# Performance work log

Measured on AMD Instinct MI355X. Metric: run time of the kernel, lower is better.

Reference implementation:

```python
import jax, jax.numpy as jnp
import numpy as np

N = 50000
E = 600000
H = 128   # hidden_channels (input to decoder)
O = 128   # output_channels (LSTM hidden size)
S = 8     # seq_len


def setup_inputs() -> dict:
    key = jax.random.key(0)
    ks = jax.random.split(key, 10)
    x = jax.random.normal(ks[0], (N, H), dtype=jnp.float32)
    c = jax.random.normal(ks[1], (N, H), dtype=jnp.float32)
    edge_index = jax.random.randint(ks[2], (2, E), 0, N, dtype=jnp.int64)
    # GCNConv weights (PyG: out = norm_agg(x @ W) + b)
    sc = lambda fan_in: 1.0 / np.sqrt(fan_in)
    Wh = jax.random.uniform(ks[3], (H, O), jnp.float32, -sc(H), sc(H))
    bh = jnp.zeros((O,), jnp.float32)
    Wc = jax.random.uniform(ks[4], (H, O), jnp.float32, -sc(H), sc(H))
    bc = jnp.zeros((O,), jnp.float32)
    # per-timestep cell convs: GCNConv(H + O, 4*O)
    Wcell = jax.random.uniform(ks[5], (S, H + O, 4 * O), jnp.float32, -sc(H + O), sc(H + O))
    bcell = jnp.zeros((S, 4 * O), jnp.float32)
    return {"x": x, "c": c, "edge_index": edge_index,
            "Wh": Wh, "bh": bh, "Wc": Wc, "bc": bc,
            "Wcell": Wcell, "bcell": bcell}


def _gcn(feat, W, b, src, dst, dinv):
    # PyG GCNConv with default add_self_loops=True, edge_weight=None:
    # out = D^{-1/2}(A+I)D^{-1/2} (feat @ W) + b
    xw = feat @ W                                   # [N, C_out]
    norm = (dinv[src] * dinv[dst])[:, None]         # [E, 1]
    agg = jax.ops.segment_sum(xw[src] * norm, dst, num_segments=N)
    agg = agg + (dinv * dinv)[:, None] * xw         # self-loop term
    return agg + b


def reference(x, c, edge_index, Wh, bh, Wc, bc, Wcell, bcell):
    src = edge_index[0]
    dst = edge_index[1]
    # degree (with self-loops, unit edge weights); computed on target index
    deg = jax.ops.segment_sum(jnp.ones((E,), jnp.float32), dst, num_segments=N) + 1.0
    dinv = 1.0 / jnp.sqrt(deg)

    h_cur = _gcn(x, Wh, bh, src, dst, dinv)
    c_cur = _gcn(c, Wc, bc, src, dst, dinv)

    def step(carry, params):
        h, cs = carry
        W, b = params
        combined = jnp.concatenate([x, h], axis=1)          # [N, H+O]
        cc = _gcn(combined, W, b, src, dst, dinv)           # [N, 4O]
        cc_f, cc_i, cc_o, cc_g = jnp.split(cc, 4, axis=1)
        f = jax.nn.sigmoid(cc_f)
        i = jax.nn.sigmoid(cc_i)
        o = jax.nn.sigmoid(cc_o)
        g = jnp.tanh(cc_g)
        c_next = f * cs + i * g
        h_next = o * jnp.tanh(c_next)
        return (h_next, c_next), h_next

    (h_fin, c_fin), hs = jax.lax.scan(step, (h_cur, c_cur), (Wcell, bcell))
    return hs, (h_fin, c_fin)  # hs: [S, N, O]
```

## Files before the change

kernel.cpp:

```cpp
#include <hip/hip_runtime.h>
#include <hip/hip_bf16.h>
#include <hip/hip_fp16.h>
#include <cstddef>


#define TPB 256

typedef __attribute__((ext_vector_type(8))) short bf16x8;
typedef __attribute__((ext_vector_type(4))) float f32x4;

__device__ __forceinline__ float sigf(float x) {
    return 1.0f / (1.0f + __expf(-x));
}
__device__ __forceinline__ float tanhfast(float x) {
    return 1.0f - 2.0f / (__expf(2.0f * x) + 1.0f);
}


__global__ void k_hist(const int* __restrict__ dst, int* __restrict__ counts, int E) {
    int e = blockIdx.x * TPB + threadIdx.x;
    if (e < E) atomicAdd(&counts[dst[e]], 1);
}

__global__ void k_scan_block(const int* __restrict__ counts, int* __restrict__ offsets,
                             int* __restrict__ sums, int N) {
    __shared__ int s[TPB];
    int tid = threadIdx.x;
    int gid = blockIdx.x * TPB + tid;
    int v = (gid < N) ? counts[gid] : 0;
    s[tid] = v;
    __syncthreads();
    for (int d = 1; d < TPB; d <<= 1) {
        int t = (tid >= d) ? s[tid - d] : 0;
        __syncthreads();
        s[tid] += t;
        __syncthreads();
    }
    if (gid < N) offsets[gid] = s[tid] - v;
    if (tid == TPB - 1) sums[blockIdx.x] = s[tid];
}

__global__ void k_scan_tops(int* __restrict__ sums, int nb) {
    __shared__ int s[TPB];
    int tid = threadIdx.x;
    int v = (tid < nb) ? sums[tid] : 0;
    s[tid] = v;
    __syncthreads();
    for (int d = 1; d < TPB; d <<= 1) {
        int t = (tid >= d) ? s[tid - d] : 0;
        __syncthreads();
        s[tid] += t;
        __syncthreads();
    }
    if (tid < nb) sums[tid] = s[tid] - v;
}

__global__ void k_scan_finish(const int* __restrict__ counts, int* __restrict__ offsets,
                              const int* __restrict__ sums, int* __restrict__ cursor,
                              float* __restrict__ dinv, int N, int E) {
    int gid = blockIdx.x * TPB + threadIdx.x;
    if (gid < N) {
        int off = offsets[gid] + sums[blockIdx.x];
        offsets[gid] = off;
        cursor[gid]  = off;
        dinv[gid]    = rsqrtf((float)(counts[gid] + 1));
    }
    if (gid == 0) offsets[N] = E;
}

__global__ void k_csr_scatter(const int* __restrict__ src, const int* __restrict__ dst,
                              const float* __restrict__ dinv, int* __restrict__ cursor,
                              int2* __restrict__ csr_sw, int E) {
    int e = blockIdx.x * TPB + threadIdx.x;
    if (e >= E) return;
    int d = dst[e], s = src[e];
    int pos = atomicAdd(&cursor[d], 1);
    int2 r;
    r.x = s;
    r.y = __float_as_int(dinv[s] * dinv[d]);
    csr_sw[pos] = r;
}


__global__ void k_f32tof16(const float* __restrict__ in, __half* __restrict__ out, int n4) {
    int i = blockIdx.x * TPB + threadIdx.x;
    if (i >= n4) return;
    float4 v = ((const float4*)in)[i];
    __half2 lo = __floats2half2_rn(v.x, v.y);
    __half2 hi = __floats2half2_rn(v.z, v.w);
    ((__half2*)out)[2 * i]     = lo;
    ((__half2*)out)[2 * i + 1] = hi;
}


union HU { f32x4 v; __half2 h[4]; };

__global__ __launch_bounds__(TPB) void k_aggregate_h(
        const __half* __restrict__ feat, __hip_bfloat16* __restrict__ agg,
        const int* __restrict__ offsets, const int2* __restrict__ sw,
        const float* __restrict__ dinv, int N) {
    int node = blockIdx.x * 4 + (threadIdx.x >> 6);
    if (node >= N) return;
    int lane = threadIdx.x & 63;
    int g = lane >> 4, t = lane & 15;
    const f32x4* f4 = (const f32x4*)feat;
    float acc[8];
    #pragma unroll
    for (int j = 0; j < 8; ++j) acc[j] = 0.f;

    int b = offsets[node], e = offsets[node + 1];
    for (int k = b; k < e; k += 4) {
        int kk = k + g;
        int kkc = (kk < e) ? kk : (e - 1);
        int2 sv = sw[kkc];
        float w = (kk < e) ? __int_as_float(sv.y) : 0.f;
        HU u;
        u.v = f4[(size_t)sv.x * 16 + t];
        #pragma unroll
        for (int j = 0; j < 4; ++j) {
            float2 vv = __half22float2(u.h[j]);
            acc[2 * j]     = fmaf(w, vv.x, acc[2 * j]);
            acc[2 * j + 1] = fmaf(w, vv.y, acc[2 * j + 1]);
        }
    }
    #pragma unroll
    for (int j = 0; j < 8; ++j) {
        acc[j] += __shfl_xor(acc[j], 16);
        acc[j] += __shfl_xor(acc[j], 32);
    }
    if (g == 0) {
        float di = dinv[node];
        float w0 = di * di;
        HU u;
        u.v = f4[(size_t)node * 16 + t];
        union { f32x4 v; __hip_bfloat162 b2[4]; } o;
        #pragma unroll
        for (int j = 0; j < 4; ++j) {
            float2 vv = __half22float2(u.h[j]);
            float ox = fmaf(w0, vv.x, acc[2 * j]);
            float oy = fmaf(w0, vv.y, acc[2 * j + 1]);
            o.b2[j].x = __float2bfloat16(ox);
            o.b2[j].y = __float2bfloat16(oy);
        }
        *(f32x4*)(agg + (size_t)node * 128 + t * 8) = o.v;
    }
}

__global__ __launch_bounds__(TPB) void k_aggregate_h2(
        const __half* __restrict__ fa, const __half* __restrict__ fb,
        __hip_bfloat16* __restrict__ aggA, __hip_bfloat16* __restrict__ aggB,
        const int* __restrict__ offsets, const int2* __restrict__ sw,
        const float* __restrict__ dinv, int N) {
    int node = blockIdx.x * 4 + (threadIdx.x >> 6);
    if (node >= N) return;
    int lane = threadIdx.x & 63;
    int g = lane >> 4, t = lane & 15;
    const f32x4* fa4 = (const f32x4*)fa;
    const f32x4* fb4 = (const f32x4*)fb;
    float accA[8], accB[8];
    #pragma unroll
    for (int j = 0; j < 8; ++j) { accA[j] = 0.f; accB[j] = 0.f; }

    int b = offsets[node], e = offsets[node + 1];
    for (int k = b; k < e; k += 4) {
        int kk = k + g;
        int kkc = (kk < e) ? kk : (e - 1);
        int2 sv = sw[kkc];
        float w = (kk < e) ? __int_as_float(sv.y) : 0.f;
        size_t ri = (size_t)sv.x * 16 + t;
        HU ua, ub;
        ua.v = fa4[ri];
        ub.v = fb4[ri];
        #pragma unroll
        for (int j = 0; j < 4; ++j) {
            float2 va = __half22float2(ua.h[j]);
            float2 vb = __half22float2(ub.h[j]);
            accA[2 * j]     = fmaf(w, va.x, accA[2 * j]);
            accA[2 * j + 1] = fmaf(w, va.y, accA[2 * j + 1]);
            accB[2 * j]     = fmaf(w, vb.x, accB[2 * j]);
            accB[2 * j + 1] = fmaf(w, vb.y, accB[2 * j + 1]);
        }
    }
    #pragma unroll
    for (int j = 0; j < 8; ++j) {
        accA[j] += __shfl_xor(accA[j], 16);
        accA[j] += __shfl_xor(accA[j], 32);
        accB[j] += __shfl_xor(accB[j], 16);
        accB[j] += __shfl_xor(accB[j], 32);
    }
    if (g == 0) {
        float di = dinv[node];
        float w0 = di * di;
        size_t ri = (size_t)node * 16 + t;
        HU ua, ub;
        ua.v = fa4[ri];
        ub.v = fb4[ri];
        union { f32x4 v; __hip_bfloat162 b2[4]; } oa, ob;
        #pragma unroll
        for (int j = 0; j < 4; ++j) {
            float2 va = __half22float2(ua.h[j]);
            float2 vb = __half22float2(ub.h[j]);
            oa.b2[j].x = __float2bfloat16(fmaf(w0, va.x, accA[2 * j]));
            oa.b2[j].y = __float2bfloat16(fmaf(w0, va.y, accA[2 * j + 1]));
            ob.b2[j].x = __float2bfloat16(fmaf(w0, vb.x, accB[2 * j]));
            ob.b2[j].y = __float2bfloat16(fmaf(w0, vb.y, accB[2 * j + 1]));
        }
        *(f32x4*)(aggA + (size_t)node * 128 + t * 8) = oa.v;
        *(f32x4*)(aggB + (size_t)node * 128 + t * 8) = ob.v;
    }
}


__global__ void k_pack_w128(const float* __restrict__ W, __hip_bfloat16* __restrict__ Wp) {
    int idx = blockIdx.x * TPB + threadIdx.x;
    if (idx >= 16384) return;
    int j = idx & 7, lane = (idx >> 3) & 63, pblk = (idx >> 9) & 7, ks = idx >> 12;
    int k = ks * 32 + (lane >> 4) * 8 + j;
    int col = pblk * 16 + (lane & 15);
    Wp[idx] = __float2bfloat16(W[k * 128 + col]);
}

__global__ void k_pack_wcell(const float* __restrict__ W, __hip_bfloat16* __restrict__ Wp, int S) {
    int idx = blockIdx.x * TPB + threadIdx.x;
    if (idx >= S * 131072) return;
    int j = idx & 7, lane = (idx >> 3) & 63, pblk = (idx >> 9) & 31;
    int ks = (idx >> 14) & 7, s = idx >> 17;
    int p = pblk * 16 + (lane & 15);
    int jcol = p >> 2, gate = p & 3;
    int k = ks * 32 + (lane >> 4) * 8 + j;
    Wp[idx] = __float2bfloat16(W[(size_t)s * 131072 + k * 512 + gate * 128 + jcol]);
}


__global__ __launch_bounds__(TPB) void k_gemm_t(
        const __hip_bfloat16* __restrict__ Ap,
        const __hip_bfloat16* __restrict__ featb,
        const float* __restrict__ bias, float* __restrict__ Cout,
        __half* __restrict__ outh, int N) {
    __shared__ __align__(16) short Bs[128 * 40];
    int tid = threadIdx.x;
    int wave = tid >> 6, lane = tid & 63;
    int w_p = wave >> 1, w_n = wave & 1;
    int n0 = blockIdx.x * 128;
    int quad = lane >> 4, m16 = lane & 15;
    f32x4 zero = {0.f, 0.f, 0.f, 0.f};
    f32x4 acc[4][4];
    #pragma unroll
    for (int t = 0; t < 4; ++t)
        #pragma unroll
        for (int g = 0; g < 4; ++g) acc[t][g] = zero;

    for (int ks = 0; ks < 4; ++ks) {
        int kbase = ks * 32;
        __syncthreads();
        #pragma unroll
        for (int it = 0; it < 2; ++it) {
            int lin = it * TPB + tid;
            int row = lin >> 2, seg = lin & 3;
            int node = n0 + row;
            f32x4 v = zero;
            if (node < N) v = *(const f32x4*)(featb + (size_t)node * 128 + kbase + seg * 8);
            *(f32x4*)&Bs[row * 40 + seg * 8] = v;
        }
        __syncthreads();
        bf16x8 a[4], b[4];
        #pragma unroll
        for (int t = 0; t < 4; ++t)
            a[t] = *(const bf16x8*)(Ap + (((size_t)ks * 8 + w_p * 4 + t) * 64 + lane) * 8);
        #pragma unroll
        for (int g = 0; g < 4; ++g)
            b[g] = *(const bf16x8*)&Bs[(w_n * 64 + g * 16 + m16) * 40 + quad * 8];
        #pragma unroll
        for (int t = 0; t < 4; ++t)
            #pragma unroll
            for (int g = 0; g < 4; ++g)
                acc[t][g] = __builtin_amdgcn_mfma_f32_16x16x32_bf16(a[t], b[g], acc[t][g], 0, 0, 0);
    }
    #pragma unroll
    for (int t = 0; t < 4; ++t) {
        int p = w_p * 64 + t * 16 + quad * 4;
        f32x4 bv = *(const f32x4*)(bias + p);
        #pragma unroll
        for (int g = 0; g < 4; ++g) {
            int nd = n0 + w_n * 64 + g * 16 + m16;
            if (nd < N) {
                f32x4 o = acc[t][g] + bv;
                if (Cout) *(f32x4*)(Cout + (size_t)nd * 128 + p) = o;
                if (outh) {
                    __half2 lo = __floats2half2_rn(o.x, o.y);
                    __half2 hi = __floats2half2_rn(o.z, o.w);
                    __half2* hp = (__half2*)(outh + (size_t)nd * 128 + p);
                    hp[0] = lo;
                    hp[1] = hi;
                }
            }
        }
    }
}


__global__ __launch_bounds__(TPB) void k_cell_t(
        const __hip_bfloat16* __restrict__ Ap,
        const __hip_bfloat16* __restrict__ axb, const __hip_bfloat16* __restrict__ ahb,
        const float* __restrict__ bias,
        float* __restrict__ cbuf, float* __restrict__ hout,
        __half* __restrict__ houth,
        float* __restrict__ hfin, int N) {
    __shared__ __align__(16) short Bs[8][128 * 40];
    int tid = threadIdx.x;
    int wave = tid >> 6, lane = tid & 63;
    int w_p = wave >> 1, w_n = wave & 1;
    int n0 = blockIdx.x * 128;
    int quad = lane >> 4, m16 = lane & 15;
    f32x4 zero = {0.f, 0.f, 0.f, 0.f};

    #pragma unroll
    for (int it = 0; it < 16; ++it) {
        int ks = it >> 1;
        int lin = ((it & 1) << 8) + tid;
        int row = lin >> 2, seg = lin & 3;
        const __hip_bfloat16* fsrc = (ks < 4) ? axb : ahb;
        int node = n0 + row;
        f32x4 v = zero;
        if (node < N) v = *(const f32x4*)(fsrc + (size_t)node * 128 + (ks & 3) * 32 + seg * 8);
        *(f32x4*)&Bs[ks][row * 40 + seg * 8] = v;
    }
    __syncthreads();

    for (int p0i = 0; p0i < 4; ++p0i) {
        f32x4 acc[4][4];
        #pragma unroll
        for (int t = 0; t < 4; ++t)
            #pragma unroll
            for (int g = 0; g < 4; ++g) acc[t][g] = zero;

        #pragma unroll
        for (int ks = 0; ks < 8; ++ks) {
            bf16x8 a[4], b[4];
            #pragma unroll
            for (int t = 0; t < 4; ++t)
                a[t] = *(const bf16x8*)(Ap + (((size_t)ks * 32 + p0i * 8 + w_p * 4 + t) * 64 + lane) * 8);
            #pragma unroll
            for (int g = 0; g < 4; ++g)
                b[g] = *(const bf16x8*)&Bs[ks][(w_n * 64 + g * 16 + m16) * 40 + quad * 8];
            #pragma unroll
            for (int t = 0; t < 4; ++t)
                #pragma unroll
                for (int g = 0; g < 4; ++g)
                    acc[t][g] = __builtin_amdgcn_mfma_f32_16x16x32_bf16(a[t], b[g], acc[t][g], 0, 0, 0);
        }

        #pragma unroll
        for (int t = 0; t < 4; ++t) {
            int p = p0i * 128 + w_p * 64 + t * 16 + quad * 4;
            int jcol = p >> 2;
            float bf = bias[jcol], bi = bias[128 + jcol], bo = bias[256 + jcol], bg = bias[384 + jcol];
            #pragma unroll
            for (int g = 0; g < 4; ++g) {
                int nd = n0 + w_n * 64 + g * 16 + m16;
                if (nd < N) {
                    float fv = sigf(acc[t][g].x + bf);
                    float iv = sigf(acc[t][g].y + bi);
                    float ov = sigf(acc[t][g].z + bo);
                    float gv = tanhfast(acc[t][g].w + bg);
                    size_t idx = (size_t)nd * 128 + jcol;
                    float cp = cbuf[idx];
                    float cn = fmaf(fv, cp, iv * gv);
                    cbuf[idx] = cn;
                    float hn = ov * tanhfast(cn);
                    hout[idx] = hn;
                    houth[idx] = __float2half(hn);
                    if (hfin) hfin[idx] = hn;
                }
            }
        }
    }
}


extern "C" void kernel_launch(void* const* d_in, const int* in_sizes, int n_in,
                              void* d_out, int out_size, void* d_ws, size_t ws_size,
                              hipStream_t stream) {
    const float* x  = (const float*)d_in[0];
    const float* c  = (const float*)d_in[1];
    const int*   ei = (const int*)d_in[2];
    const float* Wh = (const float*)d_in[3];
    const float* bh = (const float*)d_in[4];
    const float* Wc = (const float*)d_in[5];
    const float* bc = (const float*)d_in[6];
    const float* Wcell = (const float*)d_in[7];
    const float* bcell = (const float*)d_in[8];
    float* out = (float*)d_out;

    const int N = in_sizes[0] / 128;
    const int E = in_sizes[2] / 2;
    const int S = in_sizes[7] / (256 * 512);
    const int* srcp = ei;
    const int* dstp = ei + E;

    float* hs   = out;
    float* hfin = out + (size_t)S * N * 128;
    float* cbuf = hfin + (size_t)N * 128;

    char* w = (char*)d_ws;
    size_t off = 0;
    auto alloc = [&](size_t bytes) -> void* {
        void* p = w + off;
        off += (bytes + 255) & ~(size_t)255;
        return p;
    };
    int*   counts  = (int*)alloc((size_t)N * 4);
    int*   offsets = (int*)alloc((size_t)(N + 1) * 4);
    int*   cursor  = (int*)alloc((size_t)N * 4);
    int*   sums    = (int*)alloc(256 * 4);
    int2*  csr_sw  = (int2*)alloc((size_t)E * 8);
    float* dinv    = (float*)alloc((size_t)N * 4);
    __hip_bfloat16* axb = (__hip_bfloat16*)alloc((size_t)N * 128 * 2);
    __hip_bfloat16* acb = (__hip_bfloat16*)alloc((size_t)N * 128 * 2);
    __half* xh = (__half*)alloc((size_t)N * 128 * 2);
    __half* ch = (__half*)alloc((size_t)N * 128 * 2);
    __half* hh = (__half*)alloc((size_t)N * 128 * 2);
    __hip_bfloat16* WhP = (__hip_bfloat16*)alloc(16384 * 2);
    __hip_bfloat16* WcP = (__hip_bfloat16*)alloc(16384 * 2);
    __hip_bfloat16* WcellP = (__hip_bfloat16*)alloc((size_t)S * 131072 * 2);
    (void)ws_size; (void)n_in; (void)out_size;

    hipMemsetAsync(counts, 0, (size_t)N * 4, stream);
    int eblk = (E + TPB - 1) / TPB;
    int nb   = (N + TPB - 1) / TPB;
    k_hist<<<eblk, TPB, 0, stream>>>(dstp, counts, E);
    k_scan_block<<<nb, TPB, 0, stream>>>(counts, offsets, sums, N);
    k_scan_tops<<<1, TPB, 0, stream>>>(sums, nb);
    k_scan_finish<<<nb, TPB, 0, stream>>>(counts, offsets, sums, cursor, dinv, N, E);
    k_csr_scatter<<<eblk, TPB, 0, stream>>>(srcp, dstp, dinv, cursor, csr_sw, E);

    k_pack_w128<<<64, TPB, 0, stream>>>(Wh, WhP);
    k_pack_w128<<<64, TPB, 0, stream>>>(Wc, WcP);
    k_pack_wcell<<<(S * 131072 + TPB - 1) / TPB, TPB, 0, stream>>>(Wcell, WcellP, S);

    int n4 = N * 128 / 4;
    int cb = (n4 + TPB - 1) / TPB;
    k_f32tof16<<<cb, TPB, 0, stream>>>(x, xh, n4);
    k_f32tof16<<<cb, TPB, 0, stream>>>(c, ch, n4);

    int nagg = (N + 3) / 4;
    int ngt  = (N + 127) / 128;
    k_aggregate_h2<<<nagg, TPB, 0, stream>>>(xh, ch, axb, acb, offsets, csr_sw, dinv, N);
    k_gemm_t<<<ngt, TPB, 0, stream>>>(WhP, axb, bh, nullptr, hh, N);
    k_gemm_t<<<ngt, TPB, 0, stream>>>(WcP, acb, bc, cbuf, nullptr, N);

    for (int s = 0; s < S; ++s) {
        k_aggregate_h<<<nagg, TPB, 0, stream>>>(hh, acb, offsets, csr_sw, dinv, N);
        k_cell_t<<<ngt, TPB, 0, stream>>>(
            WcellP + (size_t)s * 131072, axb, acb, bcell + (size_t)s * 512,
            cbuf, hs + (size_t)s * N * 128, hh, (s == S - 1) ? hfin : nullptr, N);
    }
}
```

Measured before the change: 1.329 ms.

## Fuse per-step h aggregation into LSTM cell GEMM with ping-pong h buffers

Each timestep's neighbor aggregation of h now runs inside the cell GEMM kernel. It is written straight into swizzled LDS, so the bf16 aggregate no longer makes a round trip through global memory and one launch per step is removed. The GEMM block grows to 512 threads with 8 waves, each wave computing fewer output tiles. Double-buffered h arrays avoid read/write hazards, since other blocks read neighbor h while this step writes the new h. Grid-stride loops with fixed grid sizes replace the one-thread-per-element preprocessing launches. The cost is that gather latency now sits serially in front of the MFMA work within each block, and only about 391 blocks exist for the fused kernel.

```diff
diff --git a/kernel.cpp b/kernel.cpp
--- a/kernel.cpp
+++ b/kernel.cpp
@@ -5,6 +5,7 @@
 
 
 #define TPB 256
+#define SWZ(row) (((row) >> 2) & 3)
 
 typedef __attribute__((ext_vector_type(8))) short bf16x8;
 typedef __attribute__((ext_vector_type(4))) float f32x4;
@@ -18,8 +19,9 @@
 
 
 __global__ void k_hist(const int* __restrict__ dst, int* __restrict__ counts, int E) {
-    int e = blockIdx.x * TPB + threadIdx.x;
-    if (e < E) atomicAdd(&counts[dst[e]], 1);
+    int stride = gridDim.x * TPB;
+    for (int e = blockIdx.x * TPB + threadIdx.x; e < E; e += stride)
+        atomicAdd(&counts[dst[e]], 1);
 }
 
 __global__ void k_scan_block(const int* __restrict__ counts, int* __restrict__ offsets,
@@ -71,142 +73,96 @@
 __global__ void k_csr_scatter(const int* __restrict__ src, const int* __restrict__ dst,
                               const float* __restrict__ dinv, int* __restrict__ cursor,
                               int2* __restrict__ csr_sw, int E) {
-    int e = blockIdx.x * TPB + threadIdx.x;
-    if (e >= E) return;
-    int d = dst[e], s = src[e];
-    int pos = atomicAdd(&cursor[d], 1);
-    int2 r;
-    r.x = s;
-    r.y = __float_as_int(dinv[s] * dinv[d]);
-    csr_sw[pos] = r;
+    int stride = gridDim.x * TPB;
+    for (int e = blockIdx.x * TPB + threadIdx.x; e < E; e += stride) {
+        int d = dst[e], s = src[e];
+        int pos = atomicAdd(&cursor[d], 1);
+        int2 r;
+        r.x = s;
+        r.y = __float_as_int(dinv[s] * dinv[d]);
+        csr_sw[pos] = r;
+    }
 }
 
 
 __global__ void k_f32tof16(const float* __restrict__ in, __half* __restrict__ out, int n4) {
-    int i = blockIdx.x * TPB + threadIdx.x;
-    if (i >= n4) return;
-    float4 v = ((const float4*)in)[i];
-    __half2 lo = __floats2half2_rn(v.x, v.y);
-    __half2 hi = __floats2half2_rn(v.z, v.w);
-    ((__half2*)out)[2 * i]     = lo;
-    ((__half2*)out)[2 * i + 1] = hi;
+    int stride = gridDim.x * TPB;
+    for (int i = blockIdx.x * TPB + threadIdx.x; i < n4; i += stride) {
+        float4 v = ((const float4*)in)[i];
+        __half2 lo = __floats2half2_rn(v.x, v.y);
+        __half2 hi = __floats2half2_rn(v.z, v.w);
+        ((__half2*)out)[2 * i]     = lo;
+        ((__half2*)out)[2 * i + 1] = hi;
+    }
 }
 
 
 union HU { f32x4 v; __half2 h[4]; };
-
-__global__ __launch_bounds__(TPB) void k_aggregate_h(
-        const __half* __restrict__ feat, __hip_bfloat16* __restrict__ agg,
-        const int* __restrict__ offsets, const int2* __restrict__ sw,
-        const float* __restrict__ dinv, int N) {
-    int node = blockIdx.x * 4 + (threadIdx.x >> 6);
-    if (node >= N) return;
-    int lane = threadIdx.x & 63;
-    int g = lane >> 4, t = lane & 15;
-    const f32x4* f4 = (const f32x4*)feat;
-    float acc[8];
-    #pragma unroll
-    for (int j = 0; j < 8; ++j) acc[j] = 0.f;
-
-    int b = offsets[node], e = offsets[node + 1];
-    for (int k = b; k < e; k += 4) {
-        int kk = k + g;
-        int kkc = (kk < e) ? kk : (e - 1);
-        int2 sv = sw[kkc];
-        float w = (kk < e) ? __int_as_float(sv.y) : 0.f;
-        HU u;
-        u.v = f4[(size_t)sv.x * 16 + t];
-        #pragma unroll
-        for (int j = 0; j < 4; ++j) {
-            float2 vv = __half22float2(u.h[j]);
-            acc[2 * j]     = fmaf(w, vv.x, acc[2 * j]);
-            acc[2 * j + 1] = fmaf(w, vv.y, acc[2 * j + 1]);
-        }
-    }
-    #pragma unroll
-    for (int j = 0; j < 8; ++j) {
-        acc[j] += __shfl_xor(acc[j], 16);
-        acc[j] += __shfl_xor(acc[j], 32);
-    }
-    if (g == 0) {
-        float di = dinv[node];
-        float w0 = di * di;
-        HU u;
-        u.v = f4[(size_t)node * 16 + t];
-        union { f32x4 v; __hip_bfloat162 b2[4]; } o;
-        #pragma unroll
-        for (int j = 0; j < 4; ++j) {
-            float2 vv = __half22float2(u.h[j]);
-            float ox = fmaf(w0, vv.x, acc[2 * j]);
-            float oy = fmaf(w0, vv.y, acc[2 * j + 1]);
-            o.b2[j].x = __float2bfloat16(ox);
-            o.b2[j].y = __float2bfloat16(oy);
-        }
-        *(f32x4*)(agg + (size_t)node * 128 + t * 8) = o.v;
-    }
-}
 
 __global__ __launch_bounds__(TPB) void k_aggregate_h2(
         const __half* __restrict__ fa, const __half* __restrict__ fb,
         __hip_bfloat16* __restrict__ aggA, __hip_bfloat16* __restrict__ aggB,
         const int* __restrict__ offsets, const int2* __restrict__ sw,
         const float* __restrict__ dinv, int N) {
-    int node = blockIdx.x * 4 + (threadIdx.x >> 6);
-    if (node >= N) return;
+    int wgid = blockIdx.x * 4 + (threadIdx.x >> 6);
+    int nwaves = gridDim.x * 4;
     int lane = threadIdx.x & 63;
     int g = lane >> 4, t = lane & 15;
     const f32x4* fa4 = (const f32x4*)fa;
     const f32x4* fb4 = (const f32x4*)fb;
-    float accA[8], accB[8];
-    #pragma unroll
-    for (int j = 0; j < 8; ++j) { accA[j] = 0.f; accB[j] = 0.f; }
-
-    int b = offsets[node], e = offsets[node + 1];
-    for (int k = b; k < e; k += 4) {
-        int kk = k + g;
-        int kkc = (kk < e) ? kk : (e - 1);
-        int2 sv = sw[kkc];
-        float w = (kk < e) ? __int_as_float(sv.y) : 0.f;
-        size_t ri = (size_t)sv.x * 16 + t;
-        HU ua, ub;
-        ua.v = fa4[ri];
-        ub.v = fb4[ri];
-        #pragma unroll
-        for (int j = 0; j < 4; ++j) {
-            float2 va = __half22float2(ua.h[j]);
-            float2 vb = __half22float2(ub.h[j]);
-            accA[2 * j]     = fmaf(w, va.x, accA[2 * j]);
-            accA[2 * j + 1] = fmaf(w, va.y, accA[2 * j + 1]);
-            accB[2 * j]     = fmaf(w, vb.x, accB[2 * j]);
-            accB[2 * j + 1] = fmaf(w, vb.y, accB[2 * j + 1]);
-        }
-    }
-    #pragma unroll
-    for (int j = 0; j < 8; ++j) {
-        accA[j] += __shfl_xor(accA[j], 16);
-        accA[j] += __shfl_xor(accA[j], 32);
-        accB[j] += __shfl_xor(accB[j], 16);
-        accB[j] += __shfl_xor(accB[j], 32);
-    }
-    if (g == 0) {
-        float di = dinv[node];
-        float w0 = di * di;
-        size_t ri = (size_t)node * 16 + t;
-        HU ua, ub;
-        ua.v = fa4[ri];
-        ub.v = fb4[ri];
-        union { f32x4 v; __hip_bfloat162 b2[4]; } oa, ob;
-        #pragma unroll
-        for (int j = 0; j < 4; ++j) {
-            float2 va = __half22float2(ua.h[j]);
-            float2 vb = __half22float2(ub.h[j]);
-            oa.b2[j].x = __float2bfloat16(fmaf(w0, va.x, accA[2 * j]));
-            oa.b2[j].y = __float2bfloat16(fmaf(w0, va.y, accA[2 * j + 1]));
-            ob.b2[j].x = __float2bfloat16(fmaf(w0, vb.x, accB[2 * j]));
-            ob.b2[j].y = __float2bfloat16(fmaf(w0, vb.y, accB[2 * j + 1]));
-        }
-        *(f32x4*)(aggA + (size_t)node * 128 + t * 8) = oa.v;
-        *(f32x4*)(aggB + (size_t)node * 128 + t * 8) = ob.v;
+
+    for (int node = wgid; node < N; node += nwaves) {
+        float accA[8], accB[8];
+        #pragma unroll
+        for (int j = 0; j < 8; ++j) { accA[j] = 0.f; accB[j] = 0.f; }
+
+        int b = offsets[node], e = offsets[node + 1];
+        for (int k = b; k < e; k += 4) {
+            int kk = k + g;
+            int kkc = (kk < e) ? kk : (e - 1);
+            int2 sv = sw[kkc];
+            float w = (kk < e) ? __int_as_float(sv.y) : 0.f;
+            size_t ri = (size_t)sv.x * 16 + t;
+            HU ua, ub;
+            ua.v = fa4[ri];
+            ub.v = fb4[ri];
+            #pragma unroll
+            for (int j = 0; j < 4; ++j) {
+                float2 va = __half22float2(ua.h[j]);
+                float2 vb = __half22float2(ub.h[j]);
+                accA[2 * j]     = fmaf(w, va.x, accA[2 * j]);
+                accA[2 * j + 1] = fmaf(w, va.y, accA[2 * j + 1]);
+                accB[2 * j]     = fmaf(w, vb.x, accB[2 * j]);
+                accB[2 * j + 1] = fmaf(w, vb.y, accB[2 * j + 1]);
+            }
+        }
+        #pragma unroll
+        for (int j = 0; j < 8; ++j) {
+            accA[j] += __shfl_xor(accA[j], 16);
+            accA[j] += __shfl_xor(accA[j], 32);
+            accB[j] += __shfl_xor(accB[j], 16);
+            accB[j] += __shfl_xor(accB[j], 32);
+        }
+        if (g == 0) {
+            float di = dinv[node];
+            float w0 = di * di;
+            size_t ri = (size_t)node * 16 + t;
+            HU ua, ub;
+            ua.v = fa4[ri];
+            ub.v = fb4[ri];
+            union { f32x4 v; __hip_bfloat162 b2[4]; } oa, ob;
+            #pragma unroll
+            for (int j = 0; j < 4; ++j) {
+                float2 va = __half22float2(ua.h[j]);
+                float2 vb = __half22float2(ub.h[j]);
+                oa.b2[j].x = __float2bfloat16(fmaf(w0, va.x, accA[2 * j]));
+                oa.b2[j].y = __float2bfloat16(fmaf(w0, va.y, accA[2 * j + 1]));
+                ob.b2[j].x = __float2bfloat16(fmaf(w0, vb.x, accB[2 * j]));
+                ob.b2[j].y = __float2bfloat16(fmaf(w0, vb.y, accB[2 * j + 1]));
+            }
+            *(f32x4*)(aggA + (size_t)node * 128 + t * 8) = oa.v;
+            *(f32x4*)(aggB + (size_t)node * 128 + t * 8) = ob.v;
+        }
     }
 }
 
@@ -221,14 +177,16 @@
 }
 
 __global__ void k_pack_wcell(const float* __restrict__ W, __hip_bfloat16* __restrict__ Wp, int S) {
-    int idx = blockIdx.x * TPB + threadIdx.x;
-    if (idx >= S * 131072) return;
-    int j = idx & 7, lane = (idx >> 3) & 63, pblk = (idx >> 9) & 31;
-    int ks = (idx >> 14) & 7, s = idx >> 17;
-    int p = pblk * 16 + (lane & 15);
-    int jcol = p >> 2, gate = p & 3;
-    int k = ks * 32 + (lane >> 4) * 8 + j;
-    Wp[idx] = __float2bfloat16(W[(size_t)s * 131072 + k * 512 + gate * 128 + jcol]);
+    int total = S * 131072;
+    int stride = gridDim.x * TPB;
+    for (int idx = blockIdx.x * TPB + threadIdx.x; idx < total; idx += stride) {
+        int j = idx & 7, lane = (idx >> 3) & 63, pblk = (idx >> 9) & 31;
+        int ks = (idx >> 14) & 7, s = idx >> 17;
+        int p = pblk * 16 + (lane & 15);
+        int jcol = p >> 2, gate = p & 3;
+        int k = ks * 32 + (lane >> 4) * 8 + j;
+        Wp[idx] = __float2bfloat16(W[(size_t)s * 131072 + k * 512 + gate * 128 + jcol]);
+    }
 }
 
 
@@ -299,60 +257,119 @@
 }
 
 
-__global__ __launch_bounds__(TPB) void k_cell_t(
+__global__ __launch_bounds__(512, 4) void k_step_fused(
         const __hip_bfloat16* __restrict__ Ap,
-        const __hip_bfloat16* __restrict__ axb, const __hip_bfloat16* __restrict__ ahb,
+        const __hip_bfloat16* __restrict__ axb,
+        const __half* __restrict__ hin,
+        const int* __restrict__ offsets, const int2* __restrict__ sw,
+        const float* __restrict__ dinv,
         const float* __restrict__ bias,
         float* __restrict__ cbuf, float* __restrict__ hout,
         __half* __restrict__ houth,
         float* __restrict__ hfin, int N) {
-    __shared__ __align__(16) short Bs[8][128 * 40];
+    __shared__ __align__(16) short Bs[8][128 * 32];
     int tid = threadIdx.x;
     int wave = tid >> 6, lane = tid & 63;
-    int w_p = wave >> 1, w_n = wave & 1;
+    int w_p = wave >> 2, w_n = wave & 3;
+    w_p = wave >> 1;
+    w_n = wave & 1;
+    int quad = lane >> 4, m16 = lane & 15;
     int n0 = blockIdx.x * 128;
-    int quad = lane >> 4, m16 = lane & 15;
     f32x4 zero = {0.f, 0.f, 0.f, 0.f};
 
-    #pragma unroll
-    for (int it = 0; it < 16; ++it) {
-        int ks = it >> 1;
-        int lin = ((it & 1) << 8) + tid;
-        int row = lin >> 2, seg = lin & 3;
-        const __hip_bfloat16* fsrc = (ks < 4) ? axb : ahb;
+    {
+        int row = tid >> 2, seg = tid & 3;
         int node = n0 + row;
-        f32x4 v = zero;
-        if (node < N) v = *(const f32x4*)(fsrc + (size_t)node * 128 + (ks & 3) * 32 + seg * 8);
-        *(f32x4*)&Bs[ks][row * 40 + seg * 8] = v;
+        #pragma unroll
+        for (int ks = 0; ks < 4; ++ks) {
+            f32x4 v = zero;
+            if (node < N) v = *(const f32x4*)(axb + (size_t)node * 128 + ks * 32 + seg * 8);
+            *(f32x4*)&Bs[ks][row * 32 + ((seg ^ SWZ(row)) << 3)] = v;
+        }
+    }
+
+    {
+        const f32x4* f4 = (const f32x4*)hin;
+        int g = quad, t = m16;
+        for (int i = 0; i < 16; ++i) {
+            int r = wave * 16 + i;
+            int node = n0 + r;
+            float acc[8];
+            #pragma unroll
+            for (int j = 0; j < 8; ++j) acc[j] = 0.f;
+            if (node < N) {
+                int b0 = offsets[node], e0 = offsets[node + 1];
+                for (int k = b0; k < e0; k += 4) {
+                    int kk = k + g;
+                    int kkc = (kk < e0) ? kk : (e0 - 1);
+                    int2 sv = sw[kkc];
+                    float w = (kk < e0) ? __int_as_float(sv.y) : 0.f;
+                    HU u;
+                    u.v = f4[(size_t)sv.x * 16 + t];
+                    #pragma unroll
+                    for (int j = 0; j < 4; ++j) {
+                        float2 vv = __half22float2(u.h[j]);
+                        acc[2 * j]     = fmaf(w, vv.x, acc[2 * j]);
+                        acc[2 * j + 1] = fmaf(w, vv.y, acc[2 * j + 1]);
+                    }
+                }
+            }
+            #pragma unroll
+            for (int j = 0; j < 8; ++j) {
+                acc[j] += __shfl_xor(acc[j], 16);
+                acc[j] += __shfl_xor(acc[j], 32);
+            }
+            if (g == 0) {
+                union { f32x4 v; __hip_bfloat162 b2[4]; } o;
+                if (node < N) {
+                    float di = dinv[node];
+                    float w0 = di * di;
+                    HU u;
+                    u.v = f4[(size_t)node * 16 + t];
+                    #pragma unroll
+                    for (int j = 0; j < 4; ++j) {
+                        float2 vv = __half22float2(u.h[j]);
+                        o.b2[j].x = __float2bfloat16(fmaf(w0, vv.x, acc[2 * j]));
+                        o.b2[j].y = __float2bfloat16(fmaf(w0, vv.y, acc[2 * j + 1]));
+                    }
+                } else {
+                    o.v = zero;
+                }
+                int seg = t & 3;
+                *(f32x4*)&Bs[4 + (t >> 2)][r * 32 + ((seg ^ SWZ(r)) << 3)] = o.v;
+            }
+        }
     }
     __syncthreads();
 
     for (int p0i = 0; p0i < 4; ++p0i) {
-        f32x4 acc[4][4];
-        #pragma unroll
-        for (int t = 0; t < 4; ++t)
+        f32x4 acc[2][4];
+        #pragma unroll
+        for (int t = 0; t < 2; ++t)
             #pragma unroll
             for (int g = 0; g < 4; ++g) acc[t][g] = zero;
 
         #pragma unroll
         for (int ks = 0; ks < 8; ++ks) {
-            bf16x8 a[4], b[4];
-            #pragma unroll
-            for (int t = 0; t < 4; ++t)
-                a[t] = *(const bf16x8*)(Ap + (((size_t)ks * 32 + p0i * 8 + w_p * 4 + t) * 64 + lane) * 8);
-            #pragma unroll
-            for (int g = 0; g < 4; ++g)
-                b[g] = *(const bf16x8*)&Bs[ks][(w_n * 64 + g * 16 + m16) * 40 + quad * 8];
-            #pragma unroll
-            for (int t = 0; t < 4; ++t)
+            bf16x8 a[2], b[4];
+            #pragma unroll
+            for (int t = 0; t < 2; ++t)
+                a[t] = *(const bf16x8*)(Ap + (((size_t)ks * 32 + p0i * 8 + w_p * 2 + t) * 64 + lane) * 8);
+            #pragma unroll
+            for (int g = 0; g < 4; ++g) {
+                int row = w_n * 64 + g * 16 + m16;
+                b[g] = *(const bf16x8*)&Bs[ks][row * 32 + ((quad ^ SWZ(row)) << 3)];
+            }
+            #pragma unroll
+            for (int t = 0; t < 2; ++t)
                 #pragma unroll
                 for (int g = 0; g < 4; ++g)
                     acc[t][g] = __builtin_amdgcn_mfma_f32_16x16x32_bf16(a[t], b[g], acc[t][g], 0, 0, 0);
         }
 
         #pragma unroll
-        for (int t = 0; t < 4; ++t) {
-            int p = p0i * 128 + w_p * 64 + t * 16 + quad * 4;
+        for (int t = 0; t < 2; ++t) {
+            int p = p0i * 128 + (w_p * 2 + t) * 16 + quad * 4;
             int jcol = p >> 2;
             float bf = bias[jcol], bi = bias[128 + jcol], bo = bias[256 + jcol], bg = bias[384 + jcol];
             #pragma unroll
@@ -417,42 +434,43 @@
     float* dinv    = (float*)alloc((size_t)N * 4);
     __hip_bfloat16* axb = (__hip_bfloat16*)alloc((size_t)N * 128 * 2);
     __hip_bfloat16* acb = (__hip_bfloat16*)alloc((size_t)N * 128 * 2);
-    __half* xh = (__half*)alloc((size_t)N * 128 * 2);
-    __half* ch = (__half*)alloc((size_t)N * 128 * 2);
-    __half* hh = (__half*)alloc((size_t)N * 128 * 2);
+    __half* xh  = (__half*)alloc((size_t)N * 128 * 2);
+    __half* ch  = (__half*)alloc((size_t)N * 128 * 2);
+    __half* hhA = (__half*)alloc((size_t)N * 128 * 2);
+    __half* hhB = (__half*)alloc((size_t)N * 128 * 2);
     __hip_bfloat16* WhP = (__hip_bfloat16*)alloc(16384 * 2);
     __hip_bfloat16* WcP = (__hip_bfloat16*)alloc(16384 * 2);
     __hip_bfloat16* WcellP = (__hip_bfloat16*)alloc((size_t)S * 131072 * 2);
     (void)ws_size; (void)n_in; (void)out_size;
 
     hipMemsetAsync(counts, 0, (size_t)N * 4, stream);
-    int eblk = (E + TPB - 1) / TPB;
-    int nb   = (N + TPB - 1) / TPB;
-    k_hist<<<eblk, TPB, 0, stream>>>(dstp, counts, E);
+    int nb = (N + TPB - 1) / TPB;
+    k_hist<<<1024, TPB, 0, stream>>>(dstp, counts, E);
     k_scan_block<<<nb, TPB, 0, stream>>>(counts, offsets, sums, N);
     k_scan_tops<<<1, TPB, 0, stream>>>(sums, nb);
     k_scan_finish<<<nb, TPB, 0, stream>>>(counts, offsets, sums, cursor, dinv, N, E);
-    k_csr_scatter<<<eblk, TPB, 0, stream>>>(srcp, dstp, dinv, cursor, csr_sw, E);
+    k_csr_scatter<<<1024, TPB, 0, stream>>>(srcp, dstp, dinv, cursor, csr_sw, E);
 
     k_pack_w128<<<64, TPB, 0, stream>>>(Wh, WhP);
     k_pack_w128<<<64, TPB, 0, stream>>>(Wc, WcP);
-    k_pack_wcell<<<(S * 131072 + TPB - 1) / TPB, TPB, 0, stream>>>(Wcell, WcellP, S);
+    k_pack_wcell<<<1024, TPB, 0, stream>>>(Wcell, WcellP, S);
 
     int n4 = N * 128 / 4;
-    int cb = (n4 + TPB - 1) / TPB;
-    k_f32tof16<<<cb, TPB, 0, stream>>>(x, xh, n4);
-    k_f32tof16<<<cb, TPB, 0, stream>>>(c, ch, n4);
-
-    int nagg = (N + 3) / 4;
-    int ngt  = (N + 127) / 128;
-    k_aggregate_h2<<<nagg, TPB, 0, stream>>>(xh, ch, axb, acb, offsets, csr_sw, dinv, N);
-    k_gemm_t<<<ngt, TPB, 0, stream>>>(WhP, axb, bh, nullptr, hh, N);
+    k_f32tof16<<<1024, TPB, 0, stream>>>(x, xh, n4);
+    k_f32tof16<<<1024, TPB, 0, stream>>>(c, ch, n4);
+
+    int ngt = (N + 127) / 128;
+    k_aggregate_h2<<<2048, TPB, 0, stream>>>(xh, ch, axb, acb, offsets, csr_sw, dinv, N);
+    k_gemm_t<<<ngt, TPB, 0, stream>>>(WhP, axb, bh, nullptr, hhA, N);
     k_gemm_t<<<ngt, TPB, 0, stream>>>(WcP, acb, bc, cbuf, nullptr, N);
 
+    __half* hin = hhA;
+    __half* hnx = hhB;
     for (int s = 0; s < S; ++s) {
-        k_aggregate_h<<<nagg, TPB, 0, stream>>>(hh, acb, offsets, csr_sw, dinv, N);
-        k_cell_t<<<ngt, TPB, 0, stream>>>(
-            WcellP + (size_t)s * 131072, axb, acb, bcell + (size_t)s * 512,
-            cbuf, hs + (size_t)s * N * 128, hh, (s == S - 1) ? hfin : nullptr, N);
-    }
-}
+        k_step_fused<<<ngt, 512, 0, stream>>>(
+            WcellP + (size_t)s * 131072, axb, hin, offsets, csr_sw, dinv,
+            bcell + (size_t)s * 512, cbuf, hs + (size_t)s * N * 128, hnx,
+            (s == S - 1) ? hfin : nullptr, N);
+        __half* tmp = hin; hin = hnx; hnx = tmp;
+    }
+}
```

After: 2.332 ms. 1.75x slower.

## Use grid-stride persistent loops, merge small launches, and interleave two nodes per wave

Applied to the files above, without the earlier changes.

Converts setup and aggregation kernels to grid-stride loops with fixed grid sizes, fuses the two f32-to-f16 conversions and the two small weight packings into single launches, and makes the per-step aggregation wave process two destination nodes together so two independent gather chains are in flight. The goal is to reduce launch count and block scheduling overhead and to raise memory-level parallelism in the latency-bound gathers. In exchange, load balance across waves may worsen because degrees vary, and pairing nodes wastes lanes when their degrees differ.

```diff
diff --git a/kernel.cpp b/kernel.cpp
--- a/kernel.cpp
+++ b/kernel.cpp
@@ -18,8 +18,9 @@
 
 
 __global__ void k_hist(const int* __restrict__ dst, int* __restrict__ counts, int E) {
-    int e = blockIdx.x * TPB + threadIdx.x;
-    if (e < E) atomicAdd(&counts[dst[e]], 1);
+    int stride = gridDim.x * TPB;
+    for (int e = blockIdx.x * TPB + threadIdx.x; e < E; e += stride)
+        atomicAdd(&counts[dst[e]], 1);
 }
 
 __global__ void k_scan_block(const int* __restrict__ counts, int* __restrict__ offsets,
@@ -71,25 +72,29 @@
 __global__ void k_csr_scatter(const int* __restrict__ src, const int* __restrict__ dst,
                               const float* __restrict__ dinv, int* __restrict__ cursor,
                               int2* __restrict__ csr_sw, int E) {
-    int e = blockIdx.x * TPB + threadIdx.x;
-    if (e >= E) return;
-    int d = dst[e], s = src[e];
-    int pos = atomicAdd(&cursor[d], 1);
-    int2 r;
-    r.x = s;
-    r.y = __float_as_int(dinv[s] * dinv[d]);
-    csr_sw[pos] = r;
-}
-
-
-__global__ void k_f32tof16(const float* __restrict__ in, __half* __restrict__ out, int n4) {
-    int i = blockIdx.x * TPB + threadIdx.x;
-    if (i >= n4) return;
-    float4 v = ((const float4*)in)[i];
-    __half2 lo = __floats2half2_rn(v.x, v.y);
-    __half2 hi = __floats2half2_rn(v.z, v.w);
-    ((__half2*)out)[2 * i]     = lo;
-    ((__half2*)out)[2 * i + 1] = hi;
+    int stride = gridDim.x * TPB;
+    for (int e = blockIdx.x * TPB + threadIdx.x; e < E; e += stride) {
+        int d = dst[e], s = src[e];
+        int pos = atomicAdd(&cursor[d], 1);
+        int2 r;
+        r.x = s;
+        r.y = __float_as_int(dinv[s] * dinv[d]);
+        csr_sw[pos] = r;
+    }
+}
+
+
+__global__ void k_f32tof16_2(const float* __restrict__ a, const float* __restrict__ b,
+                             __half* __restrict__ oa, __half* __restrict__ ob, int n4) {
+    int stride = gridDim.x * TPB;
+    for (int i = blockIdx.x * TPB + threadIdx.x; i < n4; i += stride) {
+        float4 va = ((const float4*)a)[i];
+        float4 vb = ((const float4*)b)[i];
+        ((__half2*)oa)[2 * i]     = __floats2half2_rn(va.x, va.y);
+        ((__half2*)oa)[2 * i + 1] = __floats2half2_rn(va.z, va.w);
+        ((__half2*)ob)[2 * i]     = __floats2half2_rn(vb.x, vb.y);
+        ((__half2*)ob)[2 * i + 1] = __floats2half2_rn(vb.z, vb.w);
+    }
 }
 
 
@@ -99,50 +104,87 @@
         const __half* __restrict__ feat, __hip_bfloat16* __restrict__ agg,
         const int* __restrict__ offsets, const int2* __restrict__ sw,
         const float* __restrict__ dinv, int N) {
-    int node = blockIdx.x * 4 + (threadIdx.x >> 6);
-    if (node >= N) return;
+    int wid = blockIdx.x * 4 + (threadIdx.x >> 6);
+    int nw = gridDim.x * 4;
     int lane = threadIdx.x & 63;
     int g = lane >> 4, t = lane & 15;
     const f32x4* f4 = (const f32x4*)feat;
-    float acc[8];
-    #pragma unroll
-    for (int j = 0; j < 8; ++j) acc[j] = 0.f;
-
-    int b = offsets[node], e = offsets[node + 1];
-    for (int k = b; k < e; k += 4) {
-        int kk = k + g;
-        int kkc = (kk < e) ? kk : (e - 1);
-        int2 sv = sw[kkc];
-        float w = (kk < e) ? __int_as_float(sv.y) : 0.f;
-        HU u;
-        u.v = f4[(size_t)sv.x * 16 + t];
-        #pragma unroll
-        for (int j = 0; j < 4; ++j) {
-            float2 vv = __half22float2(u.h[j]);
-            acc[2 * j]     = fmaf(w, vv.x, acc[2 * j]);
-            acc[2 * j + 1] = fmaf(w, vv.y, acc[2 * j + 1]);
-        }
-    }
-    #pragma unroll
-    for (int j = 0; j < 8; ++j) {
-        acc[j] += __shfl_xor(acc[j], 16);
-        acc[j] += __shfl_xor(acc[j], 32);
-    }
-    if (g == 0) {
-        float di = dinv[node];
-        float w0 = di * di;
-        HU u;
-        u.v = f4[(size_t)node * 16 + t];
-        union { f32x4 v; __hip_bfloat162 b2[4]; } o;
-        #pragma unroll
-        for (int j = 0; j < 4; ++j) {
-            float2 vv = __half22float2(u.h[j]);
-            float ox = fmaf(w0, vv.x, acc[2 * j]);
-            float oy = fmaf(w0, vv.y, acc[2 * j + 1]);
-            o.b2[j].x = __float2bfloat16(ox);
-            o.b2[j].y = __float2bfloat16(oy);
-        }
-        *(f32x4*)(agg + (size_t)node * 128 + t * 8) = o.v;
+
+    for (int n0 = wid * 2; n0 < N; n0 += nw * 2) {
+        int n1 = n0 + 1;
+        bool has1 = (n1 < N);
+        int b0 = offsets[n0], e0 = offsets[n0 + 1];
+        int b1 = has1 ? offsets[n1] : 0;
+        int e1 = has1 ? offsets[n1 + 1] : 0;
+        int s0 = (e0 > b0) ? e0 - 1 : 0;
+        int s1 = (e1 > b1) ? e1 - 1 : 0;
+        int it0 = (e0 - b0 + 3) >> 2;
+        int it1 = (e1 - b1 + 3) >> 2;
+        int nit = it0 > it1 ? it0 : it1;
+
+        float acc0[8], acc1[8];
+        #pragma unroll
+        for (int j = 0; j < 8; ++j) { acc0[j] = 0.f; acc1[j] = 0.f; }
+
+        for (int i = 0; i < nit; ++i) {
+            int kk0 = b0 + 4 * i + g;
+            int kc0 = (kk0 < e0) ? kk0 : s0;
+            int kk1 = b1 + 4 * i + g;
+            int kc1 = (kk1 < e1) ? kk1 : s1;
+            int2 v0 = sw[kc0];
+            int2 v1 = sw[kc1];
+            float w0 = (kk0 < e0) ? __int_as_float(v0.y) : 0.f;
+            float w1 = (kk1 < e1) ? __int_as_float(v1.y) : 0.f;
+            HU u0, u1;
+            u0.v = f4[(size_t)v0.x * 16 + t];
+            u1.v = f4[(size_t)v1.x * 16 + t];
+            #pragma unroll
+            for (int j = 0; j < 4; ++j) {
+                float2 p0 = __half22float2(u0.h[j]);
+                float2 p1 = __half22float2(u1.h[j]);
+                acc0[2 * j]     = fmaf(w0, p0.x, acc0[2 * j]);
+                acc0[2 * j + 1] = fmaf(w0, p0.y, acc0[2 * j + 1]);
+                acc1[2 * j]     = fmaf(w1, p1.x, acc1[2 * j]);
+                acc1[2 * j + 1] = fmaf(w1, p1.y, acc1[2 * j + 1]);
+            }
+        }
+        #pragma unroll
+        for (int j = 0; j < 8; ++j) {
+            acc0[j] += __shfl_xor(acc0[j], 16);
+            acc0[j] += __shfl_xor(acc0[j], 32);
+            acc1[j] += __shfl_xor(acc1[j], 16);
+            acc1[j] += __shfl_xor(acc1[j], 32);
+        }
+        if (g == 0) {
+            {
+                float di = dinv[n0];
+                float w0 = di * di;
+                HU u;
+                u.v = f4[(size_t)n0 * 16 + t];
+                union { f32x4 v; __hip_bfloat162 b2[4]; } o;
+                #pragma unroll
+                for (int j = 0; j < 4; ++j) {
+                    float2 vv = __half22float2(u.h[j]);
+                    o.b2[j].x = __float2bfloat16(fmaf(w0, vv.x, acc0[2 * j]));
+                    o.b2[j].y = __float2bfloat16(fmaf(w0, vv.y, acc0[2 * j + 1]));
+                }
+                *(f32x4*)(agg + (size_t)n0 * 128 + t * 8) = o.v;
+            }
+            if (has1) {
+                float di = dinv[n1];
+                float w0 = di * di;
+                HU u;
+                u.v = f4[(size_t)n1 * 16 + t];
+                union { f32x4 v; __hip_bfloat162 b2[4]; } o;
+                #pragma unroll
+                for (int j = 0; j < 4; ++j) {
+                    float2 vv = __half22float2(u.h[j]);
+                    o.b2[j].x = __float2bfloat16(fmaf(w0, vv.x, acc1[2 * j]));
+                    o.b2[j].y = __float2bfloat16(fmaf(w0, vv.y, acc1[2 * j + 1]));
+                }
+                *(f32x4*)(agg + (size_t)n1 * 128 + t * 8) = o.v;
+            }
+        }
     }
 }
 
@@ -151,69 +193,76 @@
         __hip_bfloat16* __restrict__ aggA, __hip_bfloat16* __restrict__ aggB,
         const int* __restrict__ offsets, const int2* __restrict__ sw,
         const float* __restrict__ dinv, int N) {
-    int node = blockIdx.x * 4 + (threadIdx.x >> 6);
-    if (node >= N) return;
+    int wgid = blockIdx.x * 4 + (threadIdx.x >> 6);
+    int nwaves = gridDim.x * 4;
     int lane = threadIdx.x & 63;
     int g = lane >> 4, t = lane & 15;
     const f32x4* fa4 = (const f32x4*)fa;
     const f32x4* fb4 = (const f32x4*)fb;
-    float accA[8], accB[8];
-    #pragma unroll
-    for (int j = 0; j < 8; ++j) { accA[j] = 0.f; accB[j] = 0.f; }
-
-    int b = offsets[node], e = offsets[node + 1];
-    for (int k = b; k < e; k += 4) {
-        int kk = k + g;
-        int kkc = (kk < e) ? kk : (e - 1);
-        int2 sv = sw[kkc];
-        float w = (kk < e) ? __int_as_float(sv.y) : 0.f;
-        size_t ri = (size_t)sv.x * 16 + t;
-        HU ua, ub;
-        ua.v = fa4[ri];
-        ub.v = fb4[ri];
-        #pragma unroll
-        for (int j = 0; j < 4; ++j) {
-            float2 va = __half22float2(ua.h[j]);
-            float2 vb = __half22float2(ub.h[j]);
-            accA[2 * j]     = fmaf(w, va.x, accA[2 * j]);
-            accA[2 * j + 1] = fmaf(w, va.y, accA[2 * j + 1]);
-            accB[2 * j]     = fmaf(w, vb.x, accB[2 * j]);
-            accB[2 * j + 1] = fmaf(w, vb.y, accB[2 * j + 1]);
-        }
-    }
-    #pragma unroll
-    for (int j = 0; j < 8; ++j) {
-        accA[j] += __shfl_xor(accA[j], 16);
-        accA[j] += __shfl_xor(accA[j], 32);
-        accB[j] += __shfl_xor(accB[j], 16);
-        accB[j] += __shfl_xor(accB[j], 32);
-    }
-    if (g == 0) {
-        float di = dinv[node];
-        float w0 = di * di;
-        size_t ri = (size_t)node * 16 + t;
-        HU ua, ub;
-        ua.v = fa4[ri];
-        ub.v = fb4[ri];
-        union { f32x4 v; __hip_bfloat162 b2[4]; } oa, ob;
-        #pragma unroll
-        for (int j = 0; j < 4; ++j) {
-            float2 va = __half22float2(ua.h[j]);
-            float2 vb = __half22float2(ub.h[j]);
-            oa.b2[j].x = __float2bfloat16(fmaf(w0, va.x, accA[2 * j]));
-            oa.b2[j].y = __float2bfloat16(fmaf(w0, va.y, accA[2 * j + 1]));
-            ob.b2[j].x = __float2bfloat16(fmaf(w0, vb.x, accB[2 * j]));
-            ob.b2[j].y = __float2bfloat16(fmaf(w0, vb.y, accB[2 * j + 1]));
-        }
-        *(f32x4*)(aggA + (size_t)node * 128 + t * 8) = oa.v;
-        *(f32x4*)(aggB + (size_t)node * 128 + t * 8) = ob.v;
-    }
-}
-
-
-__global__ void k_pack_w128(const float* __restrict__ W, __hip_bfloat16* __restrict__ Wp) {
-    int idx = blockIdx.x * TPB + threadIdx.x;
-    if (idx >= 16384) return;
+
+    for (int node = wgid; node < N; node += nwaves) {
+        float accA[8], accB[8];
+        #pragma unroll
+        for (int j = 0; j < 8; ++j) { accA[j] = 0.f; accB[j] = 0.f; }
+
+        int b = offsets[node], e = offsets[node + 1];
+        for (int k = b; k < e; k += 4) {
+            int kk = k + g;
+            int kkc = (kk < e) ? kk : (e - 1);
+            int2 sv = sw[kkc];
+            float w = (kk < e) ? __int_as_float(sv.y) : 0.f;
+            size_t ri = (size_t)sv.x * 16 + t;
+            HU ua, ub;
+            ua.v = fa4[ri];
+            ub.v = fb4[ri];
+            #pragma unroll
+            for (int j = 0; j < 4; ++j) {
+                float2 va = __half22float2(ua.h[j]);
+                float2 vb = __half22float2(ub.h[j]);
+                accA[2 * j]     = fmaf(w, va.x, accA[2 * j]);
+                accA[2 * j + 1] = fmaf(w, va.y, accA[2 * j + 1]);
+                accB[2 * j]     = fmaf(w, vb.x, accB[2 * j]);
+                accB[2 * j + 1] = fmaf(w, vb.y, accB[2 * j + 1]);
+            }
+        }
+        #pragma unroll
+        for (int j = 0; j < 8; ++j) {
+            accA[j] += __shfl_xor(accA[j], 16);
+            accA[j] += __shfl_xor(accA[j], 32);
+            accB[j] += __shfl_xor(accB[j], 16);
+            accB[j] += __shfl_xor(accB[j], 32);
+        }
+        if (g == 0) {
+            float di = dinv[node];
+            float w0 = di * di;
+            size_t ri = (size_t)node * 16 + t;
+            HU ua, ub;
+            ua.v = fa4[ri];
+            ub.v = fb4[ri];
+            union { f32x4 v; __hip_bfloat162 b2[4]; } oa, ob;
+            #pragma unroll
+            for (int j = 0; j < 4; ++j) {
+                float2 va = __half22float2(ua.h[j]);
+                float2 vb = __half22float2(ub.h[j]);
+                oa.b2[j].x = __float2bfloat16(fmaf(w0, va.x, accA[2 * j]));
+                oa.b2[j].y = __float2bfloat16(fmaf(w0, va.y, accA[2 * j + 1]));
+                ob.b2[j].x = __float2bfloat16(fmaf(w0, vb.x, accB[2 * j]));
+                ob.b2[j].y = __float2bfloat16(fmaf(w0, vb.y, accB[2 * j + 1]));
+            }
+            *(f32x4*)(aggA + (size_t)node * 128 + t * 8) = oa.v;
+            *(f32x4*)(aggB + (size_t)node * 128 + t * 8) = ob.v;
+        }
+    }
+}
+
+
+__global__ void k_pack_w128_2(const float* __restrict__ Wh, const float* __restrict__ Wc,
+                              __hip_bfloat16* __restrict__ WhP, __hip_bfloat16* __restrict__ WcP) {
+    int gid = blockIdx.x * TPB + threadIdx.x;
+    if (gid >= 32768) return;
+    const float* W = (gid < 16384) ? Wh : Wc;
+    __hip_bfloat16* Wp = (gid < 16384) ? WhP : WcP;
+    int idx = gid & 16383;
     int j = idx & 7, lane = (idx >> 3) & 63, pblk = (idx >> 9) & 7, ks = idx >> 12;
     int k = ks * 32 + (lane >> 4) * 8 + j;
     int col = pblk * 16 + (lane & 15);
@@ -221,14 +270,16 @@
 }
 
 __global__ void k_pack_wcell(const float* __restrict__ W, __hip_bfloat16* __restrict__ Wp, int S) {
-    int idx = blockIdx.x * TPB + threadIdx.x;
-    if (idx >= S * 131072) return;
-    int j = idx & 7, lane = (idx >> 3) & 63, pblk = (idx >> 9) & 31;
-    int ks = (idx >> 14) & 7, s = idx >> 17;
-    int p = pblk * 16 + (lane & 15);
-    int jcol = p >> 2, gate = p & 3;
-    int k = ks * 32 + (lane >> 4) * 8 + j;
-    Wp[idx] = __float2bfloat16(W[(size_t)s * 131072 + k * 512 + gate * 128 + jcol]);
+    int total = S * 131072;
+    int stride = gridDim.x * TPB;
+    for (int idx = blockIdx.x * TPB + threadIdx.x; idx < total; idx += stride) {
+        int j = idx & 7, lane = (idx >> 3) & 63, pblk = (idx >> 9) & 31;
+        int ks = (idx >> 14) & 7, s = idx >> 17;
+        int p = pblk * 16 + (lane & 15);
+        int jcol = p >> 2, gate = p & 3;
+        int k = ks * 32 + (lane >> 4) * 8 + j;
+        Wp[idx] = __float2bfloat16(W[(size_t)s * 131072 + k * 512 + gate * 128 + jcol]);
+    }
 }
 
 
@@ -426,31 +477,26 @@
     (void)ws_size; (void)n_in; (void)out_size;
 
     hipMemsetAsync(counts, 0, (size_t)N * 4, stream);
-    int eblk = (E + TPB - 1) / TPB;
-    int nb   = (N + TPB - 1) / TPB;
-    k_hist<<<eblk, TPB, 0, stream>>>(dstp, counts, E);
+    int nb = (N + TPB - 1) / TPB;
+    k_hist<<<1024, TPB, 0, stream>>>(dstp, counts, E);
     k_scan_block<<<nb, TPB, 0, stream>>>(counts, offsets, sums, N);
     k_scan_tops<<<1, TPB, 0, stream>>>(sums, nb);
     k_scan_finish<<<nb, TPB, 0, stream>>>(counts, offsets, sums, cursor, dinv, N, E);
-    k_csr_scatter<<<eblk, TPB, 0, stream>>>(srcp, dstp, dinv, cursor, csr_sw, E);
-
-    k_pack_w128<<<64, TPB, 0, stream>>>(Wh, WhP);
-    k_pack_w128<<<64, TPB, 0, stream>>>(Wc, WcP);
-    k_pack_wcell<<<(S * 131072 + TPB - 1) / TPB, TPB, 0, stream>>>(Wcell, WcellP, S);
+    k_csr_scatter<<<1024, TPB, 0, stream>>>(srcp, dstp, dinv, cursor, csr_sw, E);
+
+    k_pack_w128_2<<<128, TPB, 0, stream>>>(Wh, Wc, WhP, WcP);
+    k_pack_wcell<<<1024, TPB, 0, stream>>>(Wcell, WcellP, S);
 
     int n4 = N * 128 / 4;
-    int cb = (n4 + TPB - 1) / TPB;
-    k_f32tof16<<<cb, TPB, 0, stream>>>(x, xh, n4);
-    k_f32tof16<<<cb, TPB, 0, stream>>>(c, ch, n4);
-
-    int nagg = (N + 3) / 4;
-    int ngt  = (N + 127) / 128;
-    k_aggregate_h2<<<nagg, TPB, 0, stream>>>(xh, ch, axb, acb, offsets, csr_sw, dinv, N);
+    k_f32tof16_2<<<1024, TPB, 0, stream>>>(x, c, xh, ch, n4);
+
+    int ngt = (N + 127) / 128;
+    k_aggregate_h2<<<2048, TPB, 0, stream>>>(xh, ch, axb, acb, offsets, csr_sw, dinv, N);
     k_gemm_t<<<ngt, TPB, 0, stream>>>(WhP, axb, bh, nullptr, hh, N);
     k_gemm_t<<<ngt, TPB, 0, stream>>>(WcP, acb, bc, cbuf, nullptr, N);
 
     for (int s = 0; s < S; ++s) {
-        k_aggregate_h<<<nagg, TPB, 0, stream>>>(hh, acb, offsets, csr_sw, dinv, N);
+        k_aggregate_h<<<2048, TPB, 0, stream>>>(hh, acb, offsets, csr_sw, dinv, N);
         k_cell_t<<<ngt, TPB, 0, stream>>>(
             WcellP + (size_t)s * 131072, axb, acb, bcell + (size_t)s * 512,
             cbuf, hs + (size_t)s * N * 128, hh, (s == S - 1) ? hfin : nullptr, N);
```

Result: faster. 1.283 ms (-3.5%).
